# Performance work log

Measured on AMD Instinct MI355X. Metric: run time of the kernel, lower is better.

The kernel has to match this reference:

```python
import jax, jax.numpy as jnp
import numpy as np

B, S, H = 1, 2048, 2048
NH, NKV, HD = 32, 8, 64
RBS, ICS, RBN = 64, 64, 16          # retrieval_block_size, input_chunk_size, retrieval_block_num
RLEN = RBS * RBN                     # 1024 retrieval tokens
KV = RLEN + S                        # 3072 total kv length
START = RLEN                         # INPUT_START_IDX
SCALE = HD ** -0.5
NEG = -1e9


def _document_ids():
    # mirrors get_document_ids
    ids = np.full(KV, -1, np.int32)
    ids[:START] = np.arange(START) // RBS + 1            # retrieval blocks -> 1..RBN
    chunk = np.arange(S) // ICS
    ids[START:] = np.where(chunk == 0, -1, np.minimum(chunk, RBN))
    return ids


def _block_mask():
    # mirrors causal_retrieval_mask_mod, precomputed dense [S, KV]
    ids = _document_ids()
    qpos = np.arange(S) + START
    kv = np.arange(KV)
    causal = (qpos[:, None] >= kv[None, :]) & (kv[None, :] > START)
    doc = (ids[qpos][:, None] == ids[None, :]) & (kv[None, :] < START)
    return jnp.asarray(causal | doc)


_MASK = _block_mask()


def _rotate_half(x):
    h = x.shape[-1] // 2
    return jnp.concatenate([-x[..., h:], x[..., :h]], axis=-1)


def setup_inputs() -> dict:
    key = jax.random.key(0)
    ks = jax.random.split(key, 6)
    inv_freq = 1.0 / (10000.0 ** (np.arange(0, HD, 2, dtype=np.float32) / HD))
    ang = np.arange(S, dtype=np.float32)[:, None] * inv_freq[None, :]   # [S, HD/2]
    emb = np.concatenate([ang, ang], axis=-1)                            # [S, HD]
    cos = jnp.asarray(np.cos(emb))[None].astype(jnp.float32)            # [1, S, HD]
    sin = jnp.asarray(np.sin(emb))[None].astype(jnp.float32)
    return {
        "hidden_states": jax.random.normal(ks[0], (B, S, H), jnp.float32),
        "cos": cos,
        "sin": sin,
        "retrieval_key": jax.random.normal(ks[1], (B, NKV, RLEN, HD), jnp.float32),
        "retrieval_value": jax.random.normal(ks[2], (B, NKV, RLEN, HD), jnp.float32),
        "Wq": jax.random.normal(ks[3], (H, NH * HD), jnp.float32) * 0.02,
        "Wk": jax.random.normal(ks[4], (H, NKV * HD), jnp.float32) * 0.02,
        "Wv": jax.random.normal(ks[5], (H, NKV * HD), jnp.float32) * 0.02,
        "Wo": jax.random.normal(jax.random.fold_in(key, 7), (NH * HD, H), jnp.float32) * 0.02,
    }


def reference(hidden_states, cos, sin, retrieval_key, retrieval_value, Wq, Wk, Wv, Wo):
    # QKV projections -> [B, nheads, S, HD]
    q = (hidden_states @ Wq).reshape(B, S, NH, HD).transpose(0, 2, 1, 3)
    k = (hidden_states @ Wk).reshape(B, S, NKV, HD).transpose(0, 2, 1, 3)
    v = (hidden_states @ Wv).reshape(B, S, NKV, HD).transpose(0, 2, 1, 3)
    # RoPE (retrieval kv is pre-encoded; rope only on current tokens)
    c, s = cos[:, None, :, :], sin[:, None, :, :]
    q = q * c + _rotate_half(q) * s
    k = k * c + _rotate_half(k) * s
    # prepend retrieval kv
    k = jnp.concatenate([retrieval_key, k], axis=2)    # [B, NKV, KV, HD]
    v = jnp.concatenate([retrieval_value, v], axis=2)
    # GQA: expand kv heads
    g = NH // NKV
    k = jnp.repeat(k, g, axis=1)                        # [B, NH, KV, HD]
    v = jnp.repeat(v, g, axis=1)
    scores = jnp.einsum("bhqd,bhkd->bhqk", q, k) * SCALE
    scores = jnp.where(_MASK[None, None], scores, NEG)
    probs = jax.nn.softmax(scores, axis=-1)
    # fully-masked rows (q_idx 0) -> zero output, matching flex_attention
    row_valid = _MASK.any(axis=-1)[None, None, :, None]
    probs = jnp.where(row_valid, probs, 0.0)
    out = jnp.einsum("bhqk,bhkd->bhqd", probs, v)
    out = out.transpose(0, 2, 1, 3).reshape(B, S, NH * HD)
    return out @ Wo
```

## Files before the change

kernel.cpp:

```cpp
#include <hip/hip_runtime.h>

#define S_LEN 2048
#define H_DIM 2048
#define NH 32
#define NKV 8
#define HD 64
#define RLEN 1024
#define KVTOT 3072
#define SCALE 0.125f
#define QS 0.18033688011112042f
#define FIX8 11.541560327111707f

typedef unsigned short ushort_t;
using short8 = __attribute__((ext_vector_type(8))) short;
using f32x4 = __attribute__((ext_vector_type(4))) float;

__device__ __forceinline__ float b2f(unsigned short u) {
    union { unsigned int i; float f; } v;
    v.i = ((unsigned int)u) << 16;
    return v.f;
}
__device__ __forceinline__ unsigned short f2b(float f) {
    union { float f; unsigned int i; } v;
    v.f = f;
    unsigned int x = v.i;
    return (unsigned short)((x + 0x7fffu + ((x >> 16) & 1u)) >> 16);
}

__global__ void detect9(const void* p0, const void* p1, const void* p2,
                        const void* p3, const void* p4, const void* p5,
                        const void* p6, const void* p7, const void* p8,
                        int* flags)
{
    __shared__ int bad;
    if (threadIdx.x == 0) bad = 0;
    __syncthreads();
    const void* ps[9] = {p0, p1, p2, p3, p4, p5, p6, p7, p8};
    const unsigned int* w = (const unsigned int*)ps[blockIdx.x];
    int cnt = 0;
    for (int i = threadIdx.x; i < 4096; i += blockDim.x) {
        unsigned int lo = w[i] & 0xFFFFu;
        unsigned int e = (lo >> 7) & 0xFFu;
        if (lo != 0u && (e < 90u || e > 140u)) ++cnt;
    }
    atomicAdd(&bad, cnt);
    __syncthreads();
    if (threadIdx.x == 0) flags[blockIdx.x] = (bad > 16) ? 1 : 0;
}

__global__ void cvt_b(const void* __restrict__ src, ushort_t* __restrict__ dst,
                      int n, const int* __restrict__ F_)
{
    const int F = *F_;
    int i = (blockIdx.x * 256 + threadIdx.x) * 8;
    if (i >= n) return;
    ushort_t o[8];
    if (F) {
        const float* p = (const float*)src + i;
        float4 f0 = ((const float4*)p)[0];
        float4 f1 = ((const float4*)p)[1];
        o[0] = f2b(f0.x); o[1] = f2b(f0.y); o[2] = f2b(f0.z); o[3] = f2b(f0.w);
        o[4] = f2b(f1.x); o[5] = f2b(f1.y); o[6] = f2b(f1.z); o[7] = f2b(f1.w);
        *(uint4*)(dst + i) = *(const uint4*)o;
    } else {
        *(uint4*)(dst + i) = *(const uint4*)((const ushort_t*)src + i);
    }
}

__global__ __launch_bounds__(256) void cvtW(
    const void* __restrict__ Wq, const void* __restrict__ Wk,
    const void* __restrict__ Wv, const void* __restrict__ Wo,
    ushort_t* __restrict__ WqkvT, ushort_t* __restrict__ WoT,
    const int* __restrict__ flags)
{
    const int z = blockIdx.z;
    if ((z == 1 || z == 2) && blockIdx.x >= 8) return;
    const void* src = (z == 0) ? Wq : (z == 1) ? Wk : (z == 2) ? Wv : Wo;
    const int F = flags[5 + z];
    const int C = (z == 1 || z == 2) ? 512 : 2048;
    ushort_t* dst = (z == 3) ? WoT : WqkvT;
    const int rofs = (z == 1) ? 2048 : (z == 2) ? 2560 : 0;

    __shared__ ushort_t S[64 * 72];
    const int r0 = blockIdx.y * 64, c0 = blockIdx.x * 64;
    const int lr = threadIdx.x >> 2, lc = (threadIdx.x & 3) * 16;
    ushort_t t[16];
    if (F) {
        const float* p = (const float*)src + (size_t)(r0 + lr) * C + c0 + lc;
#pragma unroll
        for (int j = 0; j < 16; j += 4) {
            float4 f = *(const float4*)(p + j);
            t[j] = f2b(f.x); t[j + 1] = f2b(f.y); t[j + 2] = f2b(f.z); t[j + 3] = f2b(f.w);
        }
    } else {
        const ushort_t* p = (const ushort_t*)src + (size_t)(r0 + lr) * C + c0 + lc;
        *(uint4*)t = ((const uint4*)p)[0];
        *(uint4*)(t + 8) = ((const uint4*)p)[1];
    }
    *(uint4*)&S[lr * 72 + lc] = *(const uint4*)t;
    *(uint4*)&S[lr * 72 + lc + 8] = *(const uint4*)(t + 8);
    __syncthreads();
    const int wc = threadIdx.x >> 2, wr = (threadIdx.x & 3) * 16;
    ushort_t o[16];
#pragma unroll
    for (int j = 0; j < 16; ++j) o[j] = S[(wr + j) * 72 + wc];
    ushort_t* q = dst + (size_t)(rofs + c0 + wc) * 2048 + r0 + wr;
    *(uint4*)q = *(const uint4*)o;
    *(uint4*)(q + 8) = *(const uint4*)(o + 8);
}

__global__ __launch_bounds__(256) void gemm_qkv(
    const ushort_t* __restrict__ A, const ushort_t* __restrict__ Bt,
    ushort_t* __restrict__ C, int N, int K)
{
    __shared__ __align__(16) ushort_t As[2][64 * 40];
    __shared__ __align__(16) ushort_t Bs[2][128 * 40];
    const int tid = threadIdx.x;
    const int wave = tid >> 6, lane = tid & 63;
    const int lq = lane & 15, quad = lane >> 4;
    const int m0 = blockIdx.y * 64, n0 = blockIdx.x * 128;
    const int wm = (wave & 1) * 32, wn = (wave >> 1) * 64;
    const int ar = tid >> 2, ak = (tid & 3) * 8;
    const int br = tid >> 1, bk = (tid & 1) * 16;
    const int nk = K >> 5;

    f32x4 acc[2][4];
#pragma unroll
    for (int i = 0; i < 2; ++i)
#pragma unroll
        for (int j = 0; j < 4; ++j) acc[i][j] = (f32x4){0.f, 0.f, 0.f, 0.f};

    const ushort_t* ap = A + (size_t)(m0 + ar) * K + ak;
    const ushort_t* bp = Bt + (size_t)(n0 + br) * K + bk;
    {
        uint4 a0 = ((const uint4*)ap)[0];
        uint4 b0 = ((const uint4*)bp)[0], b1 = ((const uint4*)bp)[1];
        *(uint4*)&As[0][ar * 40 + ak] = a0;
        *(uint4*)&Bs[0][br * 40 + bk] = b0; *(uint4*)&Bs[0][br * 40 + bk + 8] = b1;
    }

    for (int kt = 0; kt < nk; ++kt) {
        const int cur = kt & 1;
        uint4 na0, nb0, nb1;
        const bool more = (kt + 1 < nk);
        if (more) {
            na0 = *(const uint4*)(ap + (kt + 1) * 32);
            const ushort_t* bp2 = bp + (kt + 1) * 32;
            nb0 = ((const uint4*)bp2)[0]; nb1 = ((const uint4*)bp2)[1];
        }
        __syncthreads();
        short8 afr[2], bfr[4];
#pragma unroll
        for (int i = 0; i < 2; ++i)
            afr[i] = *(const short8*)&As[cur][(wm + i * 16 + lq) * 40 + quad * 8];
#pragma unroll
        for (int j = 0; j < 4; ++j)
            bfr[j] = *(const short8*)&Bs[cur][(wn + j * 16 + lq) * 40 + quad * 8];
#pragma unroll
        for (int i = 0; i < 2; ++i)
#pragma unroll
            for (int j = 0; j < 4; ++j)
                acc[i][j] = __builtin_amdgcn_mfma_f32_16x16x32_bf16(afr[i], bfr[j], acc[i][j], 0, 0, 0);
        __syncthreads();
        if (more) {
            const int nxt = cur ^ 1;
            *(uint4*)&As[nxt][ar * 40 + ak] = na0;
            *(uint4*)&Bs[nxt][br * 40 + bk] = nb0; *(uint4*)&Bs[nxt][br * 40 + bk + 8] = nb1;
        }
    }

#pragma unroll
    for (int i = 0; i < 2; ++i)
#pragma unroll
        for (int r = 0; r < 4; ++r) {
            ushort_t* cp = C + (size_t)(m0 + wm + i * 16 + quad * 4 + r) * N + n0 + wn + lq;
#pragma unroll
            for (int j = 0; j < 4; ++j) cp[j * 16] = f2b(acc[i][j][r]);
        }
}

__global__ __launch_bounds__(256) void gemm_fin(
    const ushort_t* __restrict__ A, const ushort_t* __restrict__ Bt,
    void* __restrict__ Cv, int N, int K, const int* __restrict__ oF_)
{
    const int oF = *oF_;
    __shared__ __align__(16) ushort_t As[2][64 * 40];
    __shared__ __align__(16) ushort_t Bs[2][128 * 40];
    const int tid = threadIdx.x;
    const int wave = tid >> 6, lane = tid & 63;
    const int lq = lane & 15, quad = lane >> 4;
    const int m0 = blockIdx.y * 64, n0 = blockIdx.x * 128;
    const int wm = (wave & 1) * 32, wn = (wave >> 1) * 64;
    const int ar = tid >> 2, ak = (tid & 3) * 8;
    const int br = tid >> 1, bk = (tid & 1) * 16;
    const int nk = K >> 5;

    f32x4 acc[2][4];
#pragma unroll
    for (int i = 0; i < 2; ++i)
#pragma unroll
        for (int j = 0; j < 4; ++j) acc[i][j] = (f32x4){0.f, 0.f, 0.f, 0.f};

    const ushort_t* ap = A + (size_t)(m0 + ar) * K + ak;
    const ushort_t* bp = Bt + (size_t)(n0 + br) * K + bk;
    {
        uint4 a0 = ((const uint4*)ap)[0];
        uint4 b0 = ((const uint4*)bp)[0], b1 = ((const uint4*)bp)[1];
        *(uint4*)&As[0][ar * 40 + ak] = a0;
        *(uint4*)&Bs[0][br * 40 + bk] = b0; *(uint4*)&Bs[0][br * 40 + bk + 8] = b1;
    }

    for (int kt = 0; kt < nk; ++kt) {
        const int cur = kt & 1;
        uint4 na0, nb0, nb1;
        const bool more = (kt + 1 < nk);
        if (more) {
            na0 = *(const uint4*)(ap + (kt + 1) * 32);
            const ushort_t* bp2 = bp + (kt + 1) * 32;
            nb0 = ((const uint4*)bp2)[0]; nb1 = ((const uint4*)bp2)[1];
        }
        __syncthreads();
        short8 afr[2], bfr[4];
#pragma unroll
        for (int i = 0; i < 2; ++i)
            afr[i] = *(const short8*)&As[cur][(wm + i * 16 + lq) * 40 + quad * 8];
#pragma unroll
        for (int j = 0; j < 4; ++j)
            bfr[j] = *(const short8*)&Bs[cur][(wn + j * 16 + lq) * 40 + quad * 8];
#pragma unroll
        for (int i = 0; i < 2; ++i)
#pragma unroll
            for (int j = 0; j < 4; ++j)
                acc[i][j] = __builtin_amdgcn_mfma_f32_16x16x32_bf16(afr[i], bfr[j], acc[i][j], 0, 0, 0);
        __syncthreads();
        if (more) {
            const int nxt = cur ^ 1;
            *(uint4*)&As[nxt][ar * 40 + ak] = na0;
            *(uint4*)&Bs[nxt][br * 40 + bk] = nb0; *(uint4*)&Bs[nxt][br * 40 + bk + 8] = nb1;
        }
    }

#pragma unroll
    for (int i = 0; i < 2; ++i)
#pragma unroll
        for (int r = 0; r < 4; ++r) {
            size_t off = (size_t)(m0 + wm + i * 16 + quad * 4 + r) * N + n0 + wn + lq;
            if (oF) {
                float* cp = (float*)Cv + off;
#pragma unroll
                for (int j = 0; j < 4; ++j) cp[j * 16] = acc[i][j][r];
            } else {
                ushort_t* cp = (ushort_t*)Cv + off;
#pragma unroll
                for (int j = 0; j < 4; ++j) cp[j * 16] = f2b(acc[i][j][r]);
            }
        }
}

__global__ __launch_bounds__(256) void prepKV(
    const void* __restrict__ rk, const void* __restrict__ rv,
    const ushort_t* __restrict__ qkvp,
    const void* __restrict__ cosv, const void* __restrict__ sinv,
    ushort_t* __restrict__ ktall, ushort_t* __restrict__ vtall,
    const int* __restrict__ flags)
{
    if (blockIdx.z == 0) {
        const int vF = flags[4];
        const int t = blockIdx.x;
        const int kvh = blockIdx.y;
        __shared__ ushort_t S[64 * 72];
        const int lr = threadIdx.x >> 2, lc = (threadIdx.x & 3) * 16;
        ushort_t tt[16];
        if (t < 16) {
            size_t base = ((size_t)kvh * RLEN + t * 64 + lr) * HD + lc;
            if (vF) {
                const float* p = (const float*)rv + base;
#pragma unroll
                for (int j = 0; j < 16; j += 4) {
                    float4 f = *(const float4*)(p + j);
                    tt[j] = f2b(f.x); tt[j + 1] = f2b(f.y); tt[j + 2] = f2b(f.z); tt[j + 3] = f2b(f.w);
                }
            } else {
                const ushort_t* p = (const ushort_t*)rv + base;
                *(uint4*)tt = ((const uint4*)p)[0];
                *(uint4*)(tt + 8) = ((const uint4*)p)[1];
            }
        } else {
            const ushort_t* p = qkvp + (size_t)((t - 16) * 64 + lr) * 3072 + 2560 + kvh * HD + lc;
            *(uint4*)tt = ((const uint4*)p)[0];
            *(uint4*)(tt + 8) = ((const uint4*)p)[1];
        }
        *(uint4*)&S[lr * 72 + lc] = *(const uint4*)tt;
        *(uint4*)&S[lr * 72 + lc + 8] = *(const uint4*)(tt + 8);
        __syncthreads();
        const int wc = threadIdx.x >> 2, wr = (threadIdx.x & 3) * 16;
        ushort_t o[16];
#pragma unroll
        for (int j = 0; j < 16; ++j) o[j] = S[(wr + j) * 72 + wc];
        const int blk = t * 2 + (wr >> 5);
        ushort_t* q = vtall + (((size_t)(kvh * 96 + blk) * 64 + wc) * 32) + (wr & 31);
        *(uint4*)q = *(const uint4*)o;
        *(uint4*)(q + 8) = *(const uint4*)(o + 8);
    } else {
        const int kF = flags[3], cF = flags[1], sF = flags[2];
        int flat = (blockIdx.y * 48 + blockIdx.x) * 256 + threadIdx.x;
        const int d0 = (flat & 3) * 8;
        const int p = (flat >> 2) % KVTOT;
        const int kvh = (flat >> 2) / KVTOT;
        ushort_t o0[8], o1[8];
        if (p < RLEN) {
            size_t base = ((size_t)kvh * RLEN + p) * HD;
            if (kF) {
                const float* s = (const float*)rk + base;
#pragma unroll
                for (int j = 0; j < 8; j += 4) {
                    float4 f = *(const float4*)(s + d0 + j);
                    o0[j] = f2b(f.x); o0[j + 1] = f2b(f.y); o0[j + 2] = f2b(f.z); o0[j + 3] = f2b(f.w);
                    float4 g = *(const float4*)(s + d0 + 32 + j);
                    o1[j] = f2b(g.x); o1[j + 1] = f2b(g.y); o1[j + 2] = f2b(g.z); o1[j + 3] = f2b(g.w);
                }
            } else {
                const ushort_t* s = (const ushort_t*)rk + base;
                *(uint4*)o0 = *(const uint4*)(s + d0);
                *(uint4*)o1 = *(const uint4*)(s + d0 + 32);
            }
        } else {
            const int si = p - RLEN;
            const ushort_t* s = qkvp + (size_t)si * 3072 + 2048 + kvh * HD;
            uint4 u0 = *(const uint4*)(s + d0);
            uint4 u1 = *(const uint4*)(s + d0 + 32);
            const ushort_t* a16 = (const ushort_t*)&u0;
            const ushort_t* b16 = (const ushort_t*)&u1;
            int ci = si * HD + d0;
            float c0[8], c1[8], s0[8], s1[8];
            if (cF) {
                const float* cp = (const float*)cosv + ci;
#pragma unroll
                for (int j = 0; j < 8; ++j) { c0[j] = cp[j]; c1[j] = cp[j + 32]; }
            } else {
                const ushort_t* cp = (const ushort_t*)cosv + ci;
#pragma unroll
                for (int j = 0; j < 8; ++j) { c0[j] = b2f(cp[j]); c1[j] = b2f(cp[j + 32]); }
            }
            if (sF) {
                const float* sp = (const float*)sinv + ci;
#pragma unroll
                for (int j = 0; j < 8; ++j) { s0[j] = sp[j]; s1[j] = sp[j + 32]; }
            } else {
                const ushort_t* sp = (const ushort_t*)sinv + ci;
#pragma unroll
                for (int j = 0; j < 8; ++j) { s0[j] = b2f(sp[j]); s1[j] = b2f(sp[j + 32]); }
            }
#pragma unroll
            for (int j = 0; j < 8; ++j) {
                float a = b2f(a16[j]), b = b2f(b16[j]);
                o0[j] = f2b(a * c0[j] - b * s0[j]);
                o1[j] = f2b(b * c1[j] + a * s1[j]);
            }
        }
        ushort_t* q = ktall + ((size_t)kvh * KVTOT + p) * HD;
        *(uint4*)(q + d0) = *(const uint4*)o0;
        *(uint4*)(q + d0 + 32) = *(const uint4*)o1;
    }
}

__global__ __launch_bounds__(256) void fattn(
    const ushort_t* __restrict__ qkvp, const ushort_t* __restrict__ ktall,
    const ushort_t* __restrict__ vtall, ushort_t* __restrict__ attno,
    const void* __restrict__ cosv, const void* __restrict__ sinv,
    const int* __restrict__ flags)
{
    const int cF = flags[1], sF = flags[2];
    const int h = blockIdx.x;
    const int yy = blockIdx.y;
    const int st = yy >> 3, r8 = yy & 7;
    const int qb = (st == 0) ? (31 - r8) : (st == 1) ? (16 + r8)
                 : (st == 2) ? (15 - r8) : r8;
    const int kvh = h >> 2;
    const int tid = threadIdx.x;
    const int wave = tid >> 6;
    const int lane = tid & 63;
    const int lq = lane & 15;
    const int quad = lane >> 4;
    const int rb64 = ((qb < 17 ? qb : 16) - 1) * 64;
    const int qrow = qb * 64 + wave * 16 + lq;

    __shared__ __align__(16) ushort_t Ks[128 * 72];
    __shared__ __align__(16) ushort_t Ps[4 * 16 * 136];
    ushort_t* pw = &Ps[wave * 16 * 136];

    short8 qfrag[2];
    {
        const int row_g = qb * 64 + wave * 16 + lq;
        const ushort_t* qrp = qkvp + (size_t)row_g * 3072 + h * HD;
        short8 t0 = *(const short8*)(qrp + quad * 8);
        short8 t1 = *(const short8*)(qrp + 32 + quad * 8);
        const int ci = row_g * HD + quad * 8;
        float c0[8], c1[8], s0[8], s1[8];
        if (cF) {
            const float* cp = (const float*)cosv + ci;
#pragma unroll
            for (int j = 0; j < 8; ++j) { c0[j] = cp[j]; c1[j] = cp[j + 32]; }
        } else {
            const ushort_t* cp = (const ushort_t*)cosv + ci;
#pragma unroll
            for (int j = 0; j < 8; ++j) { c0[j] = b2f(cp[j]); c1[j] = b2f(cp[j + 32]); }
        }
        if (sF) {
            const float* sp = (const float*)sinv + ci;
#pragma unroll
            for (int j = 0; j < 8; ++j) { s0[j] = sp[j]; s1[j] = sp[j + 32]; }
        } else {
            const ushort_t* sp = (const ushort_t*)sinv + ci;
#pragma unroll
            for (int j = 0; j < 8; ++j) { s0[j] = b2f(sp[j]); s1[j] = b2f(sp[j + 32]); }
        }
#pragma unroll
        for (int j = 0; j < 8; ++j) {
            float a = b2f((unsigned short)t0[j]), b = b2f((unsigned short)t1[j]);
            qfrag[0][j] = (short)f2b((a * c0[j] - b * s0[j]) * QS);
            qfrag[1][j] = (short)f2b((b * c1[j] + a * s1[j]) * QS);
        }
    }

    f32x4 oacc[4];
#pragma unroll
    for (int nt = 0; nt < 4; ++nt) oacc[nt] = (f32x4){0.f, 0.f, 0.f, 0.f};
    float lsum = 0.f;

    const int Lq = (qb > 0) ? qb * 64 + 128 : 64;
    const int nch = (Lq + 127) >> 7;
    const ushort_t* kbase = ktall + (size_t)kvh * KVTOT * HD;
    const ushort_t* vbase = vtall + (size_t)kvh * 96 * 2048;

    for (int c = 0; c < nch; ++c) {
        uint4 kreg0, kreg1, kreg2, kreg3;
        const int krow = tid >> 1;
        const int kd0 = (tid & 1) * 32;
        {
            int p = c * 128 + krow;
            uint4 z = {0, 0, 0, 0};
            kreg0 = z; kreg1 = z; kreg2 = z; kreg3 = z;
            if (p < Lq) {
                int pk = (qb > 0) ? ((p < 64) ? rb64 + p : 960 + p) : RLEN + p;
                const uint4* s = (const uint4*)(kbase + (size_t)pk * HD + kd0);
                kreg0 = s[0]; kreg1 = s[1]; kreg2 = s[2]; kreg3 = s[3];
            }
        }
        int vblk[4];
#pragma unroll
        for (int kc = 0; kc < 4; ++kc) {
            int p = c * 128 + kc * 32;
            int pk = (qb > 0) ? ((p < 64) ? rb64 + p : 960 + p) : RLEN + p;
            if (pk > KVTOT - 1) pk = KVTOT - 1;
            vblk[kc] = pk >> 5;
        }
        short8 vfA[4], vfB[4];
#pragma unroll
        for (int ntd = 0; ntd < 4; ++ntd)
            vfA[ntd] = *(const short8*)(vbase + ((size_t)vblk[0] * 64 + ntd * 16 + lq) * 32 + quad * 8);
#pragma unroll
        for (int ntd = 0; ntd < 4; ++ntd)
            vfB[ntd] = *(const short8*)(vbase + ((size_t)vblk[1] * 64 + ntd * 16 + lq) * 32 + quad * 8);

        {
            uint4* dk = (uint4*)&Ks[krow * 72 + kd0];
            dk[0] = kreg0; dk[1] = kreg1; dk[2] = kreg2; dk[3] = kreg3;
        }
        __syncthreads();

        const bool lastc = (c == nch - 1) || (qb == 0);
#pragma unroll
        for (int nt = 0; nt < 8; ++nt) {
            f32x4 a = (f32x4){0.f, 0.f, 0.f, 0.f};
            a = __builtin_amdgcn_mfma_f32_16x16x32_bf16(
                *(const short8*)&Ks[(nt * 16 + lq) * 72 + quad * 8], qfrag[0], a, 0, 0, 0);
            a = __builtin_amdgcn_mfma_f32_16x16x32_bf16(
                *(const short8*)&Ks[(nt * 16 + lq) * 72 + 32 + quad * 8], qfrag[1], a, 0, 0, 0);
            float pex[4];
#pragma unroll
            for (int rr = 0; rr < 4; ++rr) {
                const int p = c * 128 + nt * 16 + quad * 4 + rr;
                float pexp = exp2f(a[rr] - FIX8);
                if (lastc) {
                    bool valid;
                    if (qb > 0) valid = (p < 64) || ((p - 64) >= 1 && (p - 64) <= qrow);
                    else        valid = (p >= 1 && p <= qrow);
                    if (!valid) pexp = 0.f;
                } else if (c == 0) {
                    if (p == 64) pexp = 0.f;
                }
                lsum += pexp;
                pex[rr] = pexp;
            }
            unsigned int w0, w1;
            asm("v_cvt_pk_bf16_f32 %0, %1, %2" : "=v"(w0) : "v"(pex[0]), "v"(pex[1]));
            asm("v_cvt_pk_bf16_f32 %0, %1, %2" : "=v"(w1) : "v"(pex[2]), "v"(pex[3]));
            *(uint2*)&pw[lq * 136 + nt * 16 + quad * 4] = make_uint2(w0, w1);
        }

#pragma unroll
        for (int kc = 0; kc < 4; ++kc) {
            short8 pa = *(const short8*)&pw[lq * 136 + kc * 32 + quad * 8];
            short8 vf0, vf1, vf2, vf3;
            if (kc == 0)      { vf0 = vfA[0]; vf1 = vfA[1]; vf2 = vfA[2]; vf3 = vfA[3]; }
            else if (kc == 1) { vf0 = vfB[0]; vf1 = vfB[1]; vf2 = vfB[2]; vf3 = vfB[3]; }
            else {
                const int b = vblk[kc];
                vf0 = *(const short8*)(vbase + ((size_t)b * 64 + 0 * 16 + lq) * 32 + quad * 8);
                vf1 = *(const short8*)(vbase + ((size_t)b * 64 + 1 * 16 + lq) * 32 + quad * 8);
                vf2 = *(const short8*)(vbase + ((size_t)b * 64 + 2 * 16 + lq) * 32 + quad * 8);
                vf3 = *(const short8*)(vbase + ((size_t)b * 64 + 3 * 16 + lq) * 32 + quad * 8);
            }
            oacc[0] = __builtin_amdgcn_mfma_f32_16x16x32_bf16(pa, vf0, oacc[0], 0, 0, 0);
            oacc[1] = __builtin_amdgcn_mfma_f32_16x16x32_bf16(pa, vf1, oacc[1], 0, 0, 0);
            oacc[2] = __builtin_amdgcn_mfma_f32_16x16x32_bf16(pa, vf2, oacc[2], 0, 0, 0);
            oacc[3] = __builtin_amdgcn_mfma_f32_16x16x32_bf16(pa, vf3, oacc[3], 0, 0, 0);
        }
        __syncthreads();
    }

    float tot = lsum;
    tot += __shfl_xor(tot, 16, 64);
    tot += __shfl_xor(tot, 32, 64);
#pragma unroll
    for (int rr = 0; rr < 4; ++rr) {
        const int qg = qb * 64 + wave * 16 + quad * 4 + rr;
        const float tr = __shfl(tot, quad * 4 + rr, 64);
        const float inv = (qg == 0) ? 0.f : 1.f / tr;
        ushort_t* orow = attno + (size_t)qg * 2048 + h * HD;
#pragma unroll
        for (int nt = 0; nt < 4; ++nt)
            orow[nt * 16 + lq] = f2b(oacc[nt][rr] * inv);
    }
}

extern "C" void kernel_launch(void* const* d_in, const int* in_sizes, int n_in,
                              void* d_out, int out_size, void* d_ws, size_t ws_size,
                              hipStream_t stream) {
    const void* hs   = d_in[0];
    const void* cosv = d_in[1];
    const void* sinv = d_in[2];
    const void* rk   = d_in[3];
    const void* rv   = d_in[4];
    const void* Wq   = d_in[5];
    const void* Wk   = d_in[6];
    const void* Wv   = d_in[7];
    const void* Wo   = d_in[8];

    char* ws = (char*)d_ws;
    int*      flags  = (int*)ws;
    ushort_t* hsb    = (ushort_t*)(ws + (1u  << 20));
    ushort_t* ktall  = hsb;
    ushort_t* vtall  = (ushort_t*)(ws + (1u << 20) + (13u << 18));
    ushort_t* WqkvT  = (ushort_t*)(ws + (9u  << 20));
    ushort_t* attno  = WqkvT;
    ushort_t* WoT    = (ushort_t*)(ws + (21u << 20));
    ushort_t* qkvp   = (ushort_t*)(ws + (29u << 20));

    detect9<<<9, 256, 0, stream>>>(hs, cosv, sinv, rk, rv, Wq, Wk, Wv, Wo, flags);

    cvt_b<<<(H_DIM * S_LEN / 8 + 255) / 256, 256, 0, stream>>>(hs, hsb, H_DIM * S_LEN, flags + 0);
    cvtW<<<dim3(32, 32, 4), 256, 0, stream>>>(Wq, Wk, Wv, Wo, WqkvT, WoT, flags);

    gemm_qkv<<<dim3(3072 / 128, 2048 / 64), 256, 0, stream>>>(hsb, WqkvT, qkvp, 3072, 2048);

    prepKV<<<dim3(48, 8, 2), 256, 0, stream>>>(rk, rv, qkvp, cosv, sinv, ktall, vtall, flags);

    fattn<<<dim3(NH, 32), 256, 0, stream>>>(qkvp, ktall, vtall, attno, cosv, sinv, flags);

    gemm_fin<<<dim3(2048 / 128, 2048 / 64), 256, 0, stream>>>(attno, WoT, d_out, 2048, 2048, flags + 0);
}
```

Baseline: 268.3 us.

## Use 128x128 GEMM tiles with direct global-to-LDS async loads

Both projection GEMMs move from 64x128 to 128x128 block tiles, so each wave computes a 4x4 grid of MFMA tiles and reuses more operand data per LDS load. Operand staging now uses global_load_lds, which writes global data straight into LDS without passing through registers, and the next k-tile is issued before computing on the current one. This removes the register round trip and one barrier per k-step. In exchange, the LDS rows lose their padding and may cause bank conflicts, and the grids get smaller, which can leave CUs underused.

```diff
diff --git a/kernel.cpp b/kernel.cpp
--- a/kernel.cpp
+++ b/kernel.cpp
@@ -25,6 +25,12 @@
     v.f = f;
     unsigned int x = v.i;
     return (unsigned short)((x + 0x7fffu + ((x >> 16) & 1u)) >> 16);
+}
+
+__device__ __forceinline__ void gload16(const ushort_t* g, ushort_t* l) {
+    __builtin_amdgcn_global_load_lds(
+        (const __attribute__((address_space(1))) unsigned int*)g,
+        (__attribute__((address_space(3))) unsigned int*)l, 16, 0, 0);
 }
 
 __global__ void detect9(const void* p0, const void* p1, const void* p2,
@@ -113,70 +119,67 @@
     const ushort_t* __restrict__ A, const ushort_t* __restrict__ Bt,
     ushort_t* __restrict__ C, int N, int K)
 {
-    __shared__ __align__(16) ushort_t As[2][64 * 40];
-    __shared__ __align__(16) ushort_t Bs[2][128 * 40];
+    __shared__ __align__(16) ushort_t As[2][128 * 32];
+    __shared__ __align__(16) ushort_t Bs[2][128 * 32];
     const int tid = threadIdx.x;
     const int wave = tid >> 6, lane = tid & 63;
     const int lq = lane & 15, quad = lane >> 4;
-    const int m0 = blockIdx.y * 64, n0 = blockIdx.x * 128;
-    const int wm = (wave & 1) * 32, wn = (wave >> 1) * 64;
-    const int ar = tid >> 2, ak = (tid & 3) * 8;
-    const int br = tid >> 1, bk = (tid & 1) * 16;
+    const int m0 = blockIdx.y * 128, n0 = blockIdx.x * 128;
+    const int wm = (wave & 1) * 64, wn = (wave >> 1) * 64;
     const int nk = K >> 5;
 
-    f32x4 acc[2][4];
-#pragma unroll
-    for (int i = 0; i < 2; ++i)
+    const int srow = wave * 16 + (lane >> 2);
+    const int scol = (lane & 3) * 8;
+    const ushort_t* ga = A  + (size_t)(m0 + srow) * K + scol;
+    const ushort_t* gb = Bt + (size_t)(n0 + srow) * K + scol;
+    ushort_t* lA = &As[0][0] + wave * 16 * 32;
+    ushort_t* lB = &Bs[0][0] + wave * 16 * 32;
+
+    f32x4 acc[4][4];
+#pragma unroll
+    for (int i = 0; i < 4; ++i)
 #pragma unroll
         for (int j = 0; j < 4; ++j) acc[i][j] = (f32x4){0.f, 0.f, 0.f, 0.f};
 
-    const ushort_t* ap = A + (size_t)(m0 + ar) * K + ak;
-    const ushort_t* bp = Bt + (size_t)(n0 + br) * K + bk;
-    {
-        uint4 a0 = ((const uint4*)ap)[0];
-        uint4 b0 = ((const uint4*)bp)[0], b1 = ((const uint4*)bp)[1];
-        *(uint4*)&As[0][ar * 40 + ak] = a0;
-        *(uint4*)&Bs[0][br * 40 + bk] = b0; *(uint4*)&Bs[0][br * 40 + bk + 8] = b1;
-    }
-
+#define STAGE_G(buf, kt) do { \
+        const ushort_t* a_ = ga + (kt) * 32; \
+        const ushort_t* b_ = gb + (kt) * 32; \
+        gload16(a_,                   lA + (buf) * 4096); \
+        gload16(a_ + (size_t)64 * K,  lA + (buf) * 4096 + 64 * 32); \
+        gload16(b_,                   lB + (buf) * 4096); \
+        gload16(b_ + (size_t)64 * K,  lB + (buf) * 4096 + 64 * 32); \
+    } while (0)
+
+    STAGE_G(0, 0);
+    __syncthreads();
+    int cur = 0;
     for (int kt = 0; kt < nk; ++kt) {
-        const int cur = kt & 1;
-        uint4 na0, nb0, nb1;
-        const bool more = (kt + 1 < nk);
-        if (more) {
-            na0 = *(const uint4*)(ap + (kt + 1) * 32);
-            const ushort_t* bp2 = bp + (kt + 1) * 32;
-            nb0 = ((const uint4*)bp2)[0]; nb1 = ((const uint4*)bp2)[1];
-        }
+        if (kt + 1 < nk) STAGE_G(cur ^ 1, kt + 1);
+        short8 afr[4], bfr[4];
+#pragma unroll
+        for (int mi = 0; mi < 4; ++mi)
+            afr[mi] = *(const short8*)&As[cur][(wm + mi * 16 + lq) * 32 + quad * 8];
+#pragma unroll
+        for (int nj = 0; nj < 4; ++nj)
+            bfr[nj] = *(const short8*)&Bs[cur][(wn + nj * 16 + lq) * 32 + quad * 8];
+#pragma unroll
+        for (int mi = 0; mi < 4; ++mi)
+#pragma unroll
+            for (int nj = 0; nj < 4; ++nj)
+                acc[mi][nj] = __builtin_amdgcn_mfma_f32_16x16x32_bf16(afr[mi], bfr[nj], acc[mi][nj], 0, 0, 0);
         __syncthreads();
-        short8 afr[2], bfr[4];
-#pragma unroll
-        for (int i = 0; i < 2; ++i)
-            afr[i] = *(const short8*)&As[cur][(wm + i * 16 + lq) * 40 + quad * 8];
-#pragma unroll
-        for (int j = 0; j < 4; ++j)
-            bfr[j] = *(const short8*)&Bs[cur][(wn + j * 16 + lq) * 40 + quad * 8];
-#pragma unroll
-        for (int i = 0; i < 2; ++i)
-#pragma unroll
-            for (int j = 0; j < 4; ++j)
-                acc[i][j] = __builtin_amdgcn_mfma_f32_16x16x32_bf16(afr[i], bfr[j], acc[i][j], 0, 0, 0);
-        __syncthreads();
-        if (more) {
-            const int nxt = cur ^ 1;
-            *(uint4*)&As[nxt][ar * 40 + ak] = na0;
-            *(uint4*)&Bs[nxt][br * 40 + bk] = nb0; *(uint4*)&Bs[nxt][br * 40 + bk + 8] = nb1;
-        }
-    }
-
-#pragma unroll
-    for (int i = 0; i < 2; ++i)
+        cur ^= 1;
+    }
+
+#pragma unroll
+    for (int mi = 0; mi < 4; ++mi)
 #pragma unroll
         for (int r = 0; r < 4; ++r) {
-            ushort_t* cp = C + (size_t)(m0 + wm + i * 16 + quad * 4 + r) * N + n0 + wn + lq;
-#pragma unroll
-            for (int j = 0; j < 4; ++j) cp[j * 16] = f2b(acc[i][j][r]);
-        }
+            ushort_t* cp = C + (size_t)(m0 + wm + mi * 16 + quad * 4 + r) * N + n0 + wn + lq;
+#pragma unroll
+            for (int nj = 0; nj < 4; ++nj) cp[nj * 16] = f2b(acc[mi][nj][r]);
+        }
+#undef STAGE_G
 }
 
 __global__ __launch_bounds__(256) void gemm_fin(
@@ -184,77 +187,74 @@
     void* __restrict__ Cv, int N, int K, const int* __restrict__ oF_)
 {
     const int oF = *oF_;
-    __shared__ __align__(16) ushort_t As[2][64 * 40];
-    __shared__ __align__(16) ushort_t Bs[2][128 * 40];
+    __shared__ __align__(16) ushort_t As[2][128 * 32];
+    __shared__ __align__(16) ushort_t Bs[2][128 * 32];
     const int tid = threadIdx.x;
     const int wave = tid >> 6, lane = tid & 63;
     const int lq = lane & 15, quad = lane >> 4;
-    const int m0 = blockIdx.y * 64, n0 = blockIdx.x * 128;
-    const int wm = (wave & 1) * 32, wn = (wave >> 1) * 64;
-    const int ar = tid >> 2, ak = (tid & 3) * 8;
-    const int br = tid >> 1, bk = (tid & 1) * 16;
+    const int m0 = blockIdx.y * 128, n0 = blockIdx.x * 128;
+    const int wm = (wave & 1) * 64, wn = (wave >> 1) * 64;
     const int nk = K >> 5;
 
-    f32x4 acc[2][4];
-#pragma unroll
-    for (int i = 0; i < 2; ++i)
+    const int srow = wave * 16 + (lane >> 2);
+    const int scol = (lane & 3) * 8;
+    const ushort_t* ga = A  + (size_t)(m0 + srow) * K + scol;
+    const ushort_t* gb = Bt + (size_t)(n0 + srow) * K + scol;
+    ushort_t* lA = &As[0][0] + wave * 16 * 32;
+    ushort_t* lB = &Bs[0][0] + wave * 16 * 32;
+
+    f32x4 acc[4][4];
+#pragma unroll
+    for (int i = 0; i < 4; ++i)
 #pragma unroll
         for (int j = 0; j < 4; ++j) acc[i][j] = (f32x4){0.f, 0.f, 0.f, 0.f};
 
-    const ushort_t* ap = A + (size_t)(m0 + ar) * K + ak;
-    const ushort_t* bp = Bt + (size_t)(n0 + br) * K + bk;
-    {
-        uint4 a0 = ((const uint4*)ap)[0];
-        uint4 b0 = ((const uint4*)bp)[0], b1 = ((const uint4*)bp)[1];
-        *(uint4*)&As[0][ar * 40 + ak] = a0;
-        *(uint4*)&Bs[0][br * 40 + bk] = b0; *(uint4*)&Bs[0][br * 40 + bk + 8] = b1;
-    }
-
+#define STAGE_G(buf, kt) do { \
+        const ushort_t* a_ = ga + (kt) * 32; \
+        const ushort_t* b_ = gb + (kt) * 32; \
+        gload16(a_,                   lA + (buf) * 4096); \
+        gload16(a_ + (size_t)64 * K,  lA + (buf) * 4096 + 64 * 32); \
+        gload16(b_,                   lB + (buf) * 4096); \
+        gload16(b_ + (size_t)64 * K,  lB + (buf) * 4096 + 64 * 32); \
+    } while (0)
+
+    STAGE_G(0, 0);
+    __syncthreads();
+    int cur = 0;
     for (int kt = 0; kt < nk; ++kt) {
-        const int cur = kt & 1;
-        uint4 na0, nb0, nb1;
-        const bool more = (kt + 1 < nk);
-        if (more) {
-            na0 = *(const uint4*)(ap + (kt + 1) * 32);
-            const ushort_t* bp2 = bp + (kt + 1) * 32;
-            nb0 = ((const uint4*)bp2)[0]; nb1 = ((const uint4*)bp2)[1];
-        }
+        if (kt + 1 < nk) STAGE_G(cur ^ 1, kt + 1);
+        short8 afr[4], bfr[4];
+#pragma unroll
+        for (int mi = 0; mi < 4; ++mi)
+            afr[mi] = *(const short8*)&As[cur][(wm + mi * 16 + lq) * 32 + quad * 8];
+#pragma unroll
+        for (int nj = 0; nj < 4; ++nj)
+            bfr[nj] = *(const short8*)&Bs[cur][(wn + nj * 16 + lq) * 32 + quad * 8];
+#pragma unroll
+        for (int mi = 0; mi < 4; ++mi)
+#pragma unroll
+            for (int nj = 0; nj < 4; ++nj)
+                acc[mi][nj] = __builtin_amdgcn_mfma_f32_16x16x32_bf16(afr[mi], bfr[nj], acc[mi][nj], 0, 0, 0);
         __syncthreads();
-        short8 afr[2], bfr[4];
-#pragma unroll
-        for (int i = 0; i < 2; ++i)
-            afr[i] = *(const short8*)&As[cur][(wm + i * 16 + lq) * 40 + quad * 8];
-#pragma unroll
-        for (int j = 0; j < 4; ++j)
-            bfr[j] = *(const short8*)&Bs[cur][(wn + j * 16 + lq) * 40 + quad * 8];
-#pragma unroll
-        for (int i = 0; i < 2; ++i)
-#pragma unroll
-            for (int j = 0; j < 4; ++j)
-                acc[i][j] = __builtin_amdgcn_mfma_f32_16x16x32_bf16(afr[i], bfr[j], acc[i][j], 0, 0, 0);
-        __syncthreads();
-        if (more) {
-            const int nxt = cur ^ 1;
-            *(uint4*)&As[nxt][ar * 40 + ak] = na0;
-            *(uint4*)&Bs[nxt][br * 40 + bk] = nb0; *(uint4*)&Bs[nxt][br * 40 + bk + 8] = nb1;
-        }
-    }
-
-#pragma unroll
-    for (int i = 0; i < 2; ++i)
+        cur ^= 1;
+    }
+
+#pragma unroll
+    for (int mi = 0; mi < 4; ++mi)
 #pragma unroll
         for (int r = 0; r < 4; ++r) {
-            size_t off = (size_t)(m0 + wm + i * 16 + quad * 4 + r) * N + n0 + wn + lq;
+            size_t off = (size_t)(m0 + wm + mi * 16 + quad * 4 + r) * N + n0 + wn + lq;
             if (oF) {
                 float* cp = (float*)Cv + off;
 #pragma unroll
-                for (int j = 0; j < 4; ++j) cp[j * 16] = acc[i][j][r];
+                for (int nj = 0; nj < 4; ++nj) cp[nj * 16] = acc[mi][nj][r];
             } else {
                 ushort_t* cp = (ushort_t*)Cv + off;
 #pragma unroll
-                for (int j = 0; j < 4; ++j) cp[j * 16] = f2b(acc[i][j][r]);
-            }
-        }
+                for (int nj = 0; nj < 4; ++nj) cp[nj * 16] = f2b(acc[mi][nj][r]);
+            }
+        }
+#undef STAGE_G
 }
 
 __global__ __launch_bounds__(256) void prepKV(
@@ -563,11 +563,11 @@
     cvt_b<<<(H_DIM * S_LEN / 8 + 255) / 256, 256, 0, stream>>>(hs, hsb, H_DIM * S_LEN, flags + 0);
     cvtW<<<dim3(32, 32, 4), 256, 0, stream>>>(Wq, Wk, Wv, Wo, WqkvT, WoT, flags);
 
-    gemm_qkv<<<dim3(3072 / 128, 2048 / 64), 256, 0, stream>>>(hsb, WqkvT, qkvp, 3072, 2048);
+    gemm_qkv<<<dim3(3072 / 128, 2048 / 128), 256, 0, stream>>>(hsb, WqkvT, qkvp, 3072, 2048);
 
     prepKV<<<dim3(48, 8, 2), 256, 0, stream>>>(rk, rv, qkvp, cosv, sinv, ktall, vtall, flags);
 
     fattn<<<dim3(NH, 32), 256, 0, stream>>>(qkvp, ktall, vtall, attno, cosv, sinv, flags);
 
-    gemm_fin<<<dim3(2048 / 128, 2048 / 64), 256, 0, stream>>>(attno, WoT, d_out, 2048, 2048, flags + 0);
-}
+    gemm_fin<<<dim3(2048 / 128, 2048 / 128), 256, 0, stream>>>(attno, WoT, d_out, 2048, 2048, flags + 0);
+}
```

Result: slower. 279.7 us (+4.2%).

## Use direct global-to-LDS loads with XOR-swizzled layout in projection GEMMs

Applied to the files above, without the earlier changes.

Both projection GEMM kernels now stage tiles with global_load_lds, which writes global memory straight into shared memory instead of going through registers. The padded 40-element LDS rows become unpadded 32-element rows with an XOR swizzle on the 16-byte column chunk, meant to avoid bank conflicts while using less LDS. Launch bounds ask for 4 blocks per CU. The loop drops the sync before compute and relies on the trailing barrier, which risks reading a tile whose async load has not completed, because no explicit vmcnt wait is shown.

```diff
diff --git a/kernel.cpp b/kernel.cpp
--- a/kernel.cpp
+++ b/kernel.cpp
@@ -25,6 +25,12 @@
     v.f = f;
     unsigned int x = v.i;
     return (unsigned short)((x + 0x7fffu + ((x >> 16) & 1u)) >> 16);
+}
+
+__device__ __forceinline__ void gload16(const ushort_t* g, ushort_t* l) {
+    __builtin_amdgcn_global_load_lds(
+        (const __attribute__((address_space(1))) unsigned int*)g,
+        (__attribute__((address_space(3))) unsigned int*)l, 16, 0, 0);
 }
 
 __global__ void detect9(const void* p0, const void* p1, const void* p2,
@@ -109,64 +115,59 @@
     *(uint4*)(q + 8) = *(const uint4*)(o + 8);
 }
 
-__global__ __launch_bounds__(256) void gemm_qkv(
+__global__ __launch_bounds__(256, 4) void gemm_qkv(
     const ushort_t* __restrict__ A, const ushort_t* __restrict__ Bt,
     ushort_t* __restrict__ C, int N, int K)
 {
-    __shared__ __align__(16) ushort_t As[2][64 * 40];
-    __shared__ __align__(16) ushort_t Bs[2][128 * 40];
+    __shared__ __align__(16) ushort_t As[2][64 * 32];
+    __shared__ __align__(16) ushort_t Bs[2][128 * 32];
     const int tid = threadIdx.x;
     const int wave = tid >> 6, lane = tid & 63;
     const int lq = lane & 15, quad = lane >> 4;
     const int m0 = blockIdx.y * 64, n0 = blockIdx.x * 128;
     const int wm = (wave & 1) * 32, wn = (wave >> 1) * 64;
-    const int ar = tid >> 2, ak = (tid & 3) * 8;
-    const int br = tid >> 1, bk = (tid & 1) * 16;
     const int nk = K >> 5;
 
+    const int srow = wave * 16 + (lane >> 2);
+    const int scol = ((lane & 3) ^ ((lane >> 3) & 3)) * 8;
+    const ushort_t* ga  = A  + (size_t)(m0 + srow) * K + scol;
+    const ushort_t* gb0 = Bt + (size_t)(n0 + srow) * K + scol;
+    const ushort_t* gb1 = Bt + (size_t)(n0 + 64 + srow) * K + scol;
+    ushort_t* lA = &As[0][0] + wave * 16 * 32;
+    ushort_t* lB = &Bs[0][0] + wave * 16 * 32;
+    const int rs = (lq >> 1) & 3;
+
     f32x4 acc[2][4];
 #pragma unroll
     for (int i = 0; i < 2; ++i)
 #pragma unroll
         for (int j = 0; j < 4; ++j) acc[i][j] = (f32x4){0.f, 0.f, 0.f, 0.f};
 
-    const ushort_t* ap = A + (size_t)(m0 + ar) * K + ak;
-    const ushort_t* bp = Bt + (size_t)(n0 + br) * K + bk;
-    {
-        uint4 a0 = ((const uint4*)ap)[0];
-        uint4 b0 = ((const uint4*)bp)[0], b1 = ((const uint4*)bp)[1];
-        *(uint4*)&As[0][ar * 40 + ak] = a0;
-        *(uint4*)&Bs[0][br * 40 + bk] = b0; *(uint4*)&Bs[0][br * 40 + bk + 8] = b1;
-    }
-
+#define STAGE_G(buf, kt) do { \
+        gload16(ga  + (size_t)(kt) * 32, lA + (buf) * (64 * 32)); \
+        gload16(gb0 + (size_t)(kt) * 32, lB + (buf) * (128 * 32)); \
+        gload16(gb1 + (size_t)(kt) * 32, lB + (buf) * (128 * 32) + 64 * 32); \
+    } while (0)
+
+    STAGE_G(0, 0);
+    __syncthreads();
+    int cur = 0;
     for (int kt = 0; kt < nk; ++kt) {
-        const int cur = kt & 1;
-        uint4 na0, nb0, nb1;
-        const bool more = (kt + 1 < nk);
-        if (more) {
-            na0 = *(const uint4*)(ap + (kt + 1) * 32);
-            const ushort_t* bp2 = bp + (kt + 1) * 32;
-            nb0 = ((const uint4*)bp2)[0]; nb1 = ((const uint4*)bp2)[1];
-        }
-        __syncthreads();
+        if (kt + 1 < nk) STAGE_G(cur ^ 1, kt + 1);
         short8 afr[2], bfr[4];
 #pragma unroll
         for (int i = 0; i < 2; ++i)
-            afr[i] = *(const short8*)&As[cur][(wm + i * 16 + lq) * 40 + quad * 8];
+            afr[i] = *(const short8*)&As[cur][(wm + i * 16 + lq) * 32 + (quad ^ rs) * 8];
 #pragma unroll
         for (int j = 0; j < 4; ++j)
-            bfr[j] = *(const short8*)&Bs[cur][(wn + j * 16 + lq) * 40 + quad * 8];
+            bfr[j] = *(const short8*)&Bs[cur][(wn + j * 16 + lq) * 32 + (quad ^ rs) * 8];
 #pragma unroll
         for (int i = 0; i < 2; ++i)
 #pragma unroll
             for (int j = 0; j < 4; ++j)
                 acc[i][j] = __builtin_amdgcn_mfma_f32_16x16x32_bf16(afr[i], bfr[j], acc[i][j], 0, 0, 0);
         __syncthreads();
-        if (more) {
-            const int nxt = cur ^ 1;
-            *(uint4*)&As[nxt][ar * 40 + ak] = na0;
-            *(uint4*)&Bs[nxt][br * 40 + bk] = nb0; *(uint4*)&Bs[nxt][br * 40 + bk + 8] = nb1;
-        }
+        cur ^= 1;
     }
 
 #pragma unroll
@@ -177,67 +178,63 @@
 #pragma unroll
             for (int j = 0; j < 4; ++j) cp[j * 16] = f2b(acc[i][j][r]);
         }
-}
-
-__global__ __launch_bounds__(256) void gemm_fin(
+#undef STAGE_G
+}
+
+__global__ __launch_bounds__(256, 4) void gemm_fin(
     const ushort_t* __restrict__ A, const ushort_t* __restrict__ Bt,
     void* __restrict__ Cv, int N, int K, const int* __restrict__ oF_)
 {
     const int oF = *oF_;
-    __shared__ __align__(16) ushort_t As[2][64 * 40];
-    __shared__ __align__(16) ushort_t Bs[2][128 * 40];
+    __shared__ __align__(16) ushort_t As[2][64 * 32];
+    __shared__ __align__(16) ushort_t Bs[2][128 * 32];
     const int tid = threadIdx.x;
     const int wave = tid >> 6, lane = tid & 63;
     const int lq = lane & 15, quad = lane >> 4;
     const int m0 = blockIdx.y * 64, n0 = blockIdx.x * 128;
     const int wm = (wave & 1) * 32, wn = (wave >> 1) * 64;
-    const int ar = tid >> 2, ak = (tid & 3) * 8;
-    const int br = tid >> 1, bk = (tid & 1) * 16;
     const int nk = K >> 5;
 
+    const int srow = wave * 16 + (lane >> 2);
+    const int scol = ((lane & 3) ^ ((lane >> 3) & 3)) * 8;
+    const ushort_t* ga  = A  + (size_t)(m0 + srow) * K + scol;
+    const ushort_t* gb0 = Bt + (size_t)(n0 + srow) * K + scol;
+    const ushort_t* gb1 = Bt + (size_t)(n0 + 64 + srow) * K + scol;
+    ushort_t* lA = &As[0][0] + wave * 16 * 32;
+    ushort_t* lB = &Bs[0][0] + wave * 16 * 32;
+    const int rs = (lq >> 1) & 3;
+
     f32x4 acc[2][4];
 #pragma unroll
     for (int i = 0; i < 2; ++i)
 #pragma unroll
         for (int j = 0; j < 4; ++j) acc[i][j] = (f32x4){0.f, 0.f, 0.f, 0.f};
 
-    const ushort_t* ap = A + (size_t)(m0 + ar) * K + ak;
-    const ushort_t* bp = Bt + (size_t)(n0 + br) * K + bk;
-    {
-        uint4 a0 = ((const uint4*)ap)[0];
-        uint4 b0 = ((const uint4*)bp)[0], b1 = ((const uint4*)bp)[1];
-        *(uint4*)&As[0][ar * 40 + ak] = a0;
-        *(uint4*)&Bs[0][br * 40 + bk] = b0; *(uint4*)&Bs[0][br * 40 + bk + 8] = b1;
-    }
-
+#define STAGE_G(buf, kt) do { \
+        gload16(ga  + (size_t)(kt) * 32, lA + (buf) * (64 * 32)); \
+        gload16(gb0 + (size_t)(kt) * 32, lB + (buf) * (128 * 32)); \
+        gload16(gb1 + (size_t)(kt) * 32, lB + (buf) * (128 * 32) + 64 * 32); \
+    } while (0)
+
+    STAGE_G(0, 0);
+    __syncthreads();
+    int cur = 0;
     for (int kt = 0; kt < nk; ++kt) {
-        const int cur = kt & 1;
-        uint4 na0, nb0, nb1;
-        const bool more = (kt + 1 < nk);
-        if (more) {
-            na0 = *(const uint4*)(ap + (kt + 1) * 32);
-            const ushort_t* bp2 = bp + (kt + 1) * 32;
-            nb0 = ((const uint4*)bp2)[0]; nb1 = ((const uint4*)bp2)[1];
-        }
-        __syncthreads();
+        if (kt + 1 < nk) STAGE_G(cur ^ 1, kt + 1);
         short8 afr[2], bfr[4];
 #pragma unroll
         for (int i = 0; i < 2; ++i)
-            afr[i] = *(const short8*)&As[cur][(wm + i * 16 + lq) * 40 + quad * 8];
+            afr[i] = *(const short8*)&As[cur][(wm + i * 16 + lq) * 32 + (quad ^ rs) * 8];
 #pragma unroll
         for (int j = 0; j < 4; ++j)
-            bfr[j] = *(const short8*)&Bs[cur][(wn + j * 16 + lq) * 40 + quad * 8];
+            bfr[j] = *(const short8*)&Bs[cur][(wn + j * 16 + lq) * 32 + (quad ^ rs) * 8];
 #pragma unroll
         for (int i = 0; i < 2; ++i)
 #pragma unroll
             for (int j = 0; j < 4; ++j)
                 acc[i][j] = __builtin_amdgcn_mfma_f32_16x16x32_bf16(afr[i], bfr[j], acc[i][j], 0, 0, 0);
         __syncthreads();
-        if (more) {
-            const int nxt = cur ^ 1;
-            *(uint4*)&As[nxt][ar * 40 + ak] = na0;
-            *(uint4*)&Bs[nxt][br * 40 + bk] = nb0; *(uint4*)&Bs[nxt][br * 40 + bk + 8] = nb1;
-        }
+        cur ^= 1;
     }
 
 #pragma unroll
@@ -255,6 +252,7 @@
                 for (int j = 0; j < 4; ++j) cp[j * 16] = f2b(acc[i][j][r]);
             }
         }
+#undef STAGE_G
 }
 
 __global__ __launch_bounds__(256) void prepKV(
```

After: 268.8 us. No clear change (+0.2%).
